# Kernel tuning notes

Hardware: AMD Instinct MI355X
Metric: run time of the kernel (lower is better)

Reference implementation:

```python
import jax, jax.numpy as jnp
import numpy as np

K = 3
KK = K * K


def _offset_mask_conv(x, ow, ob):
    # Conv2d(C_in, 3*KK, k=3, stride=1, pad=1) in NCHW/OIHW
    y = jax.lax.conv_general_dilated(
        x, ow, window_strides=(1, 1), padding=((1, 1), (1, 1)),
        dimension_numbers=('NCHW', 'OIHW', 'NCHW'))
    return y + ob[None, :, None, None]


def _bilinear(xb, gy, gx):
    # xb: [C,H,W]; gy,gx: [KK,H,W] pixel coords (align_corners=True => pixel==unnormalized)
    # padding_mode='zeros': out-of-range taps contribute 0.
    C, H, W = xb.shape
    x0f = jnp.floor(gx); y0f = jnp.floor(gy)
    x0 = x0f.astype(jnp.int32); y0 = y0f.astype(jnp.int32)
    x1 = x0 + 1; y1 = y0 + 1
    wx1 = gx - x0f; wy1 = gy - y0f
    wx0 = 1.0 - wx1; wy0 = 1.0 - wy1

    def gather(yi, xi):
        valid = (yi >= 0) & (yi < H) & (xi >= 0) & (xi < W)
        yc = jnp.clip(yi, 0, H - 1)
        xc = jnp.clip(xi, 0, W - 1)
        v = xb[:, yc, xc]  # [C,KK,H,W]
        return v * valid[None].astype(xb.dtype)

    return (gather(y0, x0) * (wy0 * wx0)[None]
            + gather(y0, x1) * (wy0 * wx1)[None]
            + gather(y1, x0) * (wy1 * wx0)[None]
            + gather(y1, x1) * (wy1 * wx1)[None])  # [C,KK,H,W]


def setup_inputs() -> dict:
    key = jax.random.key(0)
    k1, k2, k3, k4 = jax.random.split(key, 4)
    B, C, Cout, H, W = 8, 64, 64, 128, 128
    x = jax.random.normal(k1, (B, C, H, W), dtype=jnp.float32)
    # offset/mask conv params (small, so offsets stay in a realistic range)
    ow = jax.random.normal(k2, (3 * KK, C, K, K), dtype=jnp.float32) * 0.01
    ob = jnp.zeros((3 * KK,), dtype=jnp.float32)
    # main conv weight (kaiming-ish scale) and bias
    w = jax.random.normal(k3, (Cout, C, K, K), dtype=jnp.float32) * (1.0 / np.sqrt(C * KK))
    b = jax.random.normal(k4, (Cout,), dtype=jnp.float32) * 0.01
    return {"x": x, "ow": ow, "ob": ob, "w": w, "b": b}


def reference(x, ow, ob, w, b):
    B, C, H, W = x.shape
    om = _offset_mask_conv(x, ow, ob)            # [B, 3*KK, H, W]
    off_x = om[:, :KK]                           # o1 -> x-offset
    off_y = om[:, KK:2 * KK]                     # o2 -> y-offset
    mask = jax.nn.sigmoid(om[:, 2 * KK:])        # [B,KK,H,W]

    gh, gw = jnp.meshgrid(jnp.arange(H, dtype=x.dtype), jnp.arange(W, dtype=x.dtype), indexing='ij')
    d = jnp.arange(-(K // 2), K // 2 + 1, dtype=x.dtype)
    kh, kw = jnp.meshgrid(d, d, indexing='ij')
    dh = kh.reshape(-1)                          # [KK] row-major (dh,dw) order matches weight[...,i,j]
    dw = kw.reshape(-1)

    gx = gw[None, None] + dw[None, :, None, None] + off_x   # [B,KK,H,W]
    gy = gh[None, None] + dh[None, :, None, None] + off_y

    sampled = jax.vmap(_bilinear)(x, gy, gx)     # [B,C,KK,H,W]
    sampled = sampled * mask[:, None]            # modulation

    wflat = w.reshape(w.shape[0], w.shape[1], KK)  # [Cout,C,KK]
    out = jnp.einsum('bckhw,ock->bohw', sampled, wflat) + b[None, :, None, None]
    return out
```

## Files before the change

kernel.cpp:

```cpp
#include <hip/hip_runtime.h>
#include <hip/hip_fp16.h>

#define B 8
#define C 64
#define H 128
#define W 128
#define HW (H * W)
#define OC 27
#define KK 9
#define COUT 64
#define KDIM 576
#define LDSROW 1152
#define NPIX 16
#define NPAIR (NPIX * KK)

typedef __attribute__((ext_vector_type(8))) short s16x8;
typedef __attribute__((ext_vector_type(4))) float f32x4;

__device__ inline ushort f2bf(float f) {
    union { float f; unsigned u; } uv;
    uv.f = f;
    unsigned r = uv.u + 0x7FFF + ((uv.u >> 16) & 1);
    return (ushort)(r >> 16);
}
__device__ inline float bf2f(ushort u) {
    return __uint_as_float((unsigned)u << 16);
}
__device__ inline unsigned pkhalf2(float a, float b) {
    __half2 h = __floats2half2_rn(a, b);
    return *(unsigned*)&h;
}

__global__ __launch_bounds__(256) void k_transpose_x(const float* __restrict__ x,
                                                     ushort* __restrict__ xTb) {
    __shared__ float lds[64][65];
    int j = blockIdx.x;
    int vb = (j & 7) * 256 + (j >> 3);
    int b = vb >> 8;
    int tile = vb & 255;
    int hw0 = tile * 64;
    int lane = threadIdx.x & 63;
    int cg = threadIdx.x >> 6;
#pragma unroll
    for (int r = 0; r < 16; ++r) {
        int c = cg * 16 + r;
        lds[c][lane] = x[(size_t)(b * C + c) * HW + hw0 + lane];
    }
    __syncthreads();
#pragma unroll
    for (int r = 0; r < 16; ++r) {
        int hwl = cg * 16 + r;
        xTb[(size_t)(b * HW + hw0 + hwl) * C + lane] = f2bf(lds[lane][hwl]);
    }
}

__global__ __launch_bounds__(256) void k_prep_w(const float* __restrict__ w,
                                                ushort* __restrict__ wB) {
    int idx = blockIdx.x * 256 + threadIdx.x;
    if (idx >= COUT * KDIM) return;
    int o = idx / KDIM;
    int Kx = idx % KDIM;
    int k = Kx >> 6;
    int c = Kx & 63;
    wB[idx] = f2bf(w[(size_t)(o * C + c) * KK + k]);
}

__global__ __launch_bounds__(256) void k_prep_aw(const float* __restrict__ ow,
                                                 ushort* __restrict__ awB) {
    int idx = blockIdx.x * 256 + threadIdx.x;
    if (idx >= 32 * KDIM) return;
    int o = idx / KDIM;
    int Kx = idx % KDIM;
    int tap = Kx >> 6;
    int c = Kx & 63;
    float v = (o < OC) ? ow[((size_t)o * C + c) * KK + tap] : 0.0f;
    awB[idx] = f2bf(v);
}

__global__ __launch_bounds__(256) void k_om(const ushort* __restrict__ xTb,
                                            const ushort* __restrict__ awB,
                                            const float* __restrict__ ob,
                                            float* __restrict__ om_pm) {
    __shared__ __align__(16) char xwin[3 * 66 * 128];
    int tid = threadIdx.x;
    int lane = tid & 63;
    int wv = tid >> 6;
    int j = blockIdx.x;
    int vb = (j & 7) * 256 + (j >> 3);
    int b = vb >> 8;
    int h = (vb >> 1) & 127;
    int w0 = (vb & 1) * 64;

    const ushort* xb = xTb + (size_t)b * (HW * C);
    int ch2 = tid & 31;
#pragma unroll
    for (int it = 0; it < 25; ++it) {
        int pi = it * 8 + (tid >> 5);
        if (pi < 198) {
            int row = pi / 66;
            int col = pi - row * 66;
            int y = h - 1 + row;
            int xc = w0 - 1 + col;
            unsigned v = 0;
            if ((unsigned)y < H && (unsigned)xc < W)
                v = *(const unsigned*)(xb + ((size_t)(y * W + xc) << 6) + ch2 * 2);
            int byte = (pi * 128 + ch2 * 4) ^ ((col & 7) << 4);
            *(unsigned*)(xwin + byte) = v;
        }
    }
    __syncthreads();

    f32x4 acc0 = {0.f, 0.f, 0.f, 0.f};
    f32x4 acc1 = {0.f, 0.f, 0.f, 0.f};
    int pixl = lane & 15;
    int q = lane >> 4;
    int base_col = wv * 16 + pixl;
    const ushort* a0 = awB + (size_t)pixl * KDIM + q * 8;
    const ushort* a1 = awB + (size_t)(16 + pixl) * KDIM + q * 8;
#pragma unroll
    for (int s = 0; s < 18; ++s) {
        int tap = s >> 1;
        int row = tap / 3;
        int cs = tap - row * 3;
        int col = base_col + cs;
        int c0b = ((s & 1) * 32 + q * 8) * 2;
        int byte = (((row * 66 + col) << 7) + c0b) ^ ((col & 7) << 4);
        s16x8 bfrag = *(const s16x8*)(xwin + byte);
        s16x8 af0 = *(const s16x8*)(a0 + s * 32);
        s16x8 af1 = *(const s16x8*)(a1 + s * 32);
        acc0 = __builtin_amdgcn_mfma_f32_16x16x32_bf16(af0, bfrag, acc0, 0, 0, 0);
        acc1 = __builtin_amdgcn_mfma_f32_16x16x32_bf16(af1, bfrag, acc1, 0, 0, 0);
    }

    __syncthreads();
    float* omt = (float*)xwin;
    {
        int pix = wv * 16 + pixl;
#pragma unroll
        for (int jj = 0; jj < 4; ++jj) {
            int oc = q * 4 + jj;
            omt[pix * 29 + oc] = acc0[jj] + ob[oc];
        }
#pragma unroll
        for (int jj = 0; jj < 4; ++jj) {
            int oc1 = 16 + q * 4 + jj;
            if (oc1 < OC) omt[pix * 29 + oc1] = acc1[jj] + ob[oc1];
        }
    }
    __syncthreads();

    float* dst = om_pm + ((size_t)b * HW + h * W + w0) * 32;
#pragma unroll
    for (int t = tid; t < 64 * 32; t += 256) {
        int pix = t >> 5;
        int oc = t & 31;
        float v = (oc < OC) ? omt[pix * 29 + oc] : 0.0f;
        dst[(size_t)pix * 32 + oc] = v;
    }
}

__global__ __launch_bounds__(256) void k_main(const ushort* __restrict__ xTb,
                                              const float* __restrict__ om_pm,
                                              const ushort* __restrict__ wB,
                                              const float* __restrict__ bias,
                                              float* __restrict__ out) {
    __shared__ __align__(16) char smem[NPIX * LDSROW];
    __shared__ uint2 mw_lds[NPAIR];
    __shared__ ushort2 mo_lds[NPAIR];

    int tid = threadIdx.x;
    int lane = tid & 63;
    int wv = tid >> 6;
    int jb = blockIdx.x;
    int vb = (jb & 7) * 1024 + (jb >> 3);
    int pb = vb * NPIX;
    int b = pb >> 14;
    int rem = pb & (HW - 1);
    int h = rem >> 7;
    int w0 = rem & (W - 1);

    if (tid < NPAIR) {
        int pix = tid / 9;
        int k = tid - pix * 9;
        const float* o0 = om_pm + ((size_t)b * HW + rem + pix) * 32;
        float offx = o0[k];
        float offy = o0[9 + k];
        float mlog = o0[18 + k];
        int dh = k / 3 - 1;
        int dw = k % 3 - 1;
        float mask = 1.0f / (1.0f + __expf(-mlog));
        float gx = (float)(w0 + pix + dw) + offx;
        float gy = (float)(h + dh) + offy;
        float x0f = floorf(gx), y0f = floorf(gy);
        int x0 = (int)x0f, y0 = (int)y0f;
        int x1 = x0 + 1, y1 = y0 + 1;
        float wx1 = gx - x0f, wy1 = gy - y0f;
        float wx0 = 1.0f - wx1, wy0 = 1.0f - wy1;
        float rw0 = ((unsigned)y0 < H) ? wy0 * mask : 0.0f;
        float rw1 = ((unsigned)y1 < H) ? wy1 * mask : 0.0f;
        int y0c = min(max(y0, 0), H - 1), y1c = min(max(y1, 0), H - 1);
        int colbase = min(max(x0, 0), W - 2);
        float cw0 = 0.0f, cw1 = 0.0f;
        if ((unsigned)x0 < W) { if (x0 == colbase) cw0 += wx0; else cw1 += wx0; }
        if ((unsigned)x1 < W) { if (x1 == colbase) cw0 += wx1; else cw1 += wx1; }
        mw_lds[tid] = make_uint2(pkhalf2(rw0 * cw0, rw0 * cw1),
                                 pkhalf2(rw1 * cw0, rw1 * cw1));
        mo_lds[tid] = make_ushort2((ushort)(((y0c * W + colbase) * (C * 2)) >> 7),
                                   (ushort)(((y1c * W + colbase) * (C * 2)) >> 7));
    }
    __syncthreads();

    const char* xbase = (const char*)(xTb + (size_t)b * (HW * C));
    bool lo_half = lane < 32;
#pragma unroll 1
    for (int pp = 0; pp < 4; ++pp) {
        int p = wv * 4 + pp;
        uint2 mwv[KK];
        int mo0[KK], mo1[KK];
#pragma unroll
        for (int k = 0; k < KK; ++k) {
            mwv[k] = mw_lds[p * 9 + k];
            ushort2 mo = mo_lds[p * 9 + k];
            mo0[k] = (int)mo.x << 7;
            mo1[k] = (int)mo.y << 7;
        }
        unsigned d0[KK], d1[KK];
#pragma unroll
        for (int k = 0; k < KK; ++k) {
            d0[k] = *(const unsigned*)(xbase + mo0[k] + lane * 4);
            d1[k] = *(const unsigned*)(xbase + mo1[k] + lane * 4);
        }
        __builtin_amdgcn_sched_barrier(0);
        int vlds = p * LDSROW + (((lane & 31) * 4) ^ ((p & 7) << 4));
#pragma unroll
        for (int k = 0; k < KK; ++k) {
            __half2 h0 = *(__half2*)&mwv[k].x;
            __half2 h1 = *(__half2*)&mwv[k].y;
            float wa = lo_half ? __half2float(h0.x) : __half2float(h0.y);
            float wb_ = lo_half ? __half2float(h1.x) : __half2float(h1.y);
            float a0 = __uint_as_float(d0[k] << 16);
            float a1 = __uint_as_float(d0[k] & 0xFFFF0000u);
            float b0 = __uint_as_float(d1[k] << 16);
            float b1 = __uint_as_float(d1[k] & 0xFFFF0000u);
            float p0 = a0 * wa + b0 * wb_;
            float p1 = a1 * wa + b1 * wb_;
            float q0 = __shfl_xor(p0, 32, 64);
            float q1 = __shfl_xor(p1, 32, 64);
            float s0 = p0 + q0, s1 = p1 + q1;
            unsigned pk;
            asm("v_cvt_pk_bf16_f32 %0, %1, %2" : "=v"(pk) : "v"(s0), "v"(s1));
            if (lane < 32) *(unsigned*)(smem + vlds + k * 128) = pk;
        }
    }
    __syncthreads();

    f32x4 acc;
#pragma unroll
    for (int j = 0; j < 4; ++j) acc[j] = bias[wv * 16 + (lane >> 4) * 4 + j];

    int pix = lane & 15;
    const ushort* wrow = wB + (size_t)(wv * 16 + pix) * KDIM + (lane >> 4) * 8;
#pragma unroll
    for (int s = 0; s < 18; ++s) {
        int kbyte = s * 64 + (lane >> 4) * 16;
        int byte = (pix * LDSROW + kbyte) ^ ((pix & 7) << 4);
        s16x8 bfrag = *(const s16x8*)(smem + byte);
        s16x8 afrag = *(const s16x8*)(wrow + s * 32);
        acc = __builtin_amdgcn_mfma_f32_16x16x32_bf16(afrag, bfrag, acc, 0, 0, 0);
    }

    float* obase = out + ((size_t)(b * COUT + wv * 16 + (lane >> 4) * 4) * HW) + h * W + w0;
#pragma unroll
    for (int j = 0; j < 4; ++j) obase[(size_t)j * HW + pix] = acc[j];
}

extern "C" void kernel_launch(void* const* d_in, const int* in_sizes, int n_in,
                              void* d_out, int out_size, void* d_ws, size_t ws_size,
                              hipStream_t stream) {
    const float* x = (const float*)d_in[0];
    const float* ow = (const float*)d_in[1];
    const float* ob = (const float*)d_in[2];
    const float* w = (const float*)d_in[3];
    const float* bias = (const float*)d_in[4];
    float* out = (float*)d_out;

    float* om_pm = (float*)d_ws;
    ushort* xTb = (ushort*)(om_pm + (size_t)B * HW * 32);
    ushort* wB = xTb + (size_t)B * HW * C;
    ushort* awB = wB + (size_t)COUT * KDIM;

    hipLaunchKernelGGL(k_transpose_x, dim3(B * 256), dim3(256), 0, stream, x, xTb);
    hipLaunchKernelGGL(k_prep_w, dim3((COUT * KDIM + 255) / 256), dim3(256), 0,
                       stream, w, wB);
    hipLaunchKernelGGL(k_prep_aw, dim3((32 * KDIM + 255) / 256), dim3(256), 0,
                       stream, ow, awB);
    hipLaunchKernelGGL(k_om, dim3(B * H * 2), dim3(256), 0, stream, xTb, awB, ob, om_pm);
    hipLaunchKernelGGL(k_main, dim3(B * HW / NPIX), dim3(256), 0, stream,
                       xTb, om_pm, wB, bias, out);
}
```

Measured before the change: 162.5 us.

## Stage input neighborhood window in LDS for deformable bilinear gathers

Each block now cooperatively loads a 5x22 pixel window of the bf16 NHWC input (all 64 channels) into shared memory, then serves bilinear sample taps from LDS when they fall inside the window. Taps outside fall back to global loads, flagged by a high bit in the packed offset. This removes the repeated scattered global reads of overlapping neighborhoods, at the cost of about 14 KB of extra LDS per block, a per-tap branch, and loss of the batched-load and sched_barrier structure that previously overlapped the global loads.

New measurement: 192.0 us. +18.2%, slower.

```diff
diff --git a/kernel.cpp b/kernel.cpp
--- a/kernel.cpp
+++ b/kernel.cpp
@@ -13,6 +13,10 @@
 #define LDSROW 1152
 #define NPIX 16
 #define NPAIR (NPIX * KK)
+#define WROWS 5
+#define WCOLS 22
+#define WRSTRIDE (WCOLS * 128)
+#define WBYTES (WROWS * WRSTRIDE)
 
 typedef __attribute__((ext_vector_type(8))) short s16x8;
 typedef __attribute__((ext_vector_type(4))) float f32x4;
@@ -165,6 +169,7 @@
                                               const float* __restrict__ bias,
                                               float* __restrict__ out) {
     __shared__ __align__(16) char smem[NPIX * LDSROW];
+    __shared__ __align__(16) char win[WBYTES];
     __shared__ uint2 mw_lds[NPAIR];
     __shared__ ushort2 mo_lds[NPAIR];
 
@@ -178,6 +183,27 @@
     int rem = pb & (HW - 1);
     int h = rem >> 7;
     int w0 = rem & (W - 1);
+
+    const char* xbase = (const char*)(xTb + (size_t)b * (HW * C));
+
+    {
+        int y0w = h - 2, c0w = w0 - 3;
+#pragma unroll
+        for (int i = 0; i < 4; ++i) {
+            int idx = i * 256 + tid;
+            if (idx < WROWS * WCOLS * 8) {
+                int wrow = idx / (WCOLS * 8);
+                int rem16 = idx - wrow * (WCOLS * 8);
+                int wcol = rem16 >> 3;
+                int ch16 = rem16 & 7;
+                int y = y0w + wrow, cx = c0w + wcol;
+                uint4 v = make_uint4(0, 0, 0, 0);
+                if ((unsigned)y < H && (unsigned)cx < W)
+                    v = *(const uint4*)(xbase + (((y << 7) + cx) << 7) + ch16 * 16);
+                *(uint4*)(win + wrow * WRSTRIDE + wcol * 128 + ch16 * 16) = v;
+            }
+        }
+    }
 
     if (tid < NPAIR) {
         int pix = tid / 9;
@@ -205,43 +231,45 @@
         if ((unsigned)x1 < W) { if (x1 == colbase) cw0 += wx1; else cw1 += wx1; }
         mw_lds[tid] = make_uint2(pkhalf2(rw0 * cw0, rw0 * cw1),
                                  pkhalf2(rw1 * cw0, rw1 * cw1));
-        mo_lds[tid] = make_ushort2((ushort)(((y0c * W + colbase) * (C * 2)) >> 7),
-                                   (ushort)(((y1c * W + colbase) * (C * 2)) >> 7));
-    }
-    __syncthreads();
-
-    const char* xbase = (const char*)(xTb + (size_t)b * (HW * C));
+        int iy0w = y0c - (h - 2), iy1w = y1c - (h - 2), icw = colbase - (w0 - 3);
+        bool inw = ((unsigned)iy0w < WROWS) && ((unsigned)iy1w < WROWS) &&
+                   ((unsigned)icw <= WCOLS - 2);
+        if (inw) {
+            mo_lds[tid] = make_ushort2((ushort)(iy0w * WRSTRIDE + icw * 128),
+                                       (ushort)(iy1w * WRSTRIDE + icw * 128));
+        } else {
+            mo_lds[tid] = make_ushort2(
+                (ushort)(0x8000u | (unsigned)((y0c << 7) + colbase)),
+                (ushort)((y1c << 7) + colbase));
+        }
+    }
+    __syncthreads();
+
     bool lo_half = lane < 32;
 #pragma unroll 1
     for (int pp = 0; pp < 4; ++pp) {
         int p = wv * 4 + pp;
-        uint2 mwv[KK];
-        int mo0[KK], mo1[KK];
+        int vlds = p * LDSROW + (((lane & 31) * 4) ^ ((p & 7) << 4));
 #pragma unroll
         for (int k = 0; k < KK; ++k) {
-            mwv[k] = mw_lds[p * 9 + k];
+            uint2 mwv = mw_lds[p * 9 + k];
             ushort2 mo = mo_lds[p * 9 + k];
-            mo0[k] = (int)mo.x << 7;
-            mo1[k] = (int)mo.y << 7;
-        }
-        unsigned d0[KK], d1[KK];
-#pragma unroll
-        for (int k = 0; k < KK; ++k) {
-            d0[k] = *(const unsigned*)(xbase + mo0[k] + lane * 4);
-            d1[k] = *(const unsigned*)(xbase + mo1[k] + lane * 4);
-        }
-        __builtin_amdgcn_sched_barrier(0);
-        int vlds = p * LDSROW + (((lane & 31) * 4) ^ ((p & 7) << 4));
-#pragma unroll
-        for (int k = 0; k < KK; ++k) {
-            __half2 h0 = *(__half2*)&mwv[k].x;
-            __half2 h1 = *(__half2*)&mwv[k].y;
+            unsigned d0, d1;
+            if (mo.x & 0x8000u) {
+                d0 = *(const unsigned*)(xbase + ((int)(mo.x & 0x7FFFu) << 7) + lane * 4);
+                d1 = *(const unsigned*)(xbase + ((int)mo.y << 7) + lane * 4);
+            } else {
+                d0 = *(const unsigned*)(win + mo.x + lane * 4);
+                d1 = *(const unsigned*)(win + mo.y + lane * 4);
+            }
+            __half2 h0 = *(__half2*)&mwv.x;
+            __half2 h1 = *(__half2*)&mwv.y;
             float wa = lo_half ? __half2float(h0.x) : __half2float(h0.y);
             float wb_ = lo_half ? __half2float(h1.x) : __half2float(h1.y);
-            float a0 = __uint_as_float(d0[k] << 16);
-            float a1 = __uint_as_float(d0[k] & 0xFFFF0000u);
-            float b0 = __uint_as_float(d1[k] << 16);
-            float b1 = __uint_as_float(d1[k] & 0xFFFF0000u);
+            float a0 = __uint_as_float(d0 << 16);
+            float a1 = __uint_as_float(d0 & 0xFFFF0000u);
+            float b0 = __uint_as_float(d1 << 16);
+            float b1 = __uint_as_float(d1 & 0xFFFF0000u);
             float p0 = a0 * wa + b0 * wb_;
             float p1 = a1 * wa + b1 * wb_;
             float q0 = __shfl_xor(p0, 32, 64);
```
